# Optimization experiments

Measured on AMD Instinct MI355X. Metric: run time of the kernel, lower is better.

Reference implementation:

```python
import jax, jax.numpy as jnp
import numpy as np

R, H, E = 200000, 256, 100000  # num_relations, hidden_dim, num_hyperedges


def setup_inputs() -> dict:
    key = jax.random.key(0)
    ks = jax.random.split(key, 8)
    rng = np.random.default_rng(0)
    # ragged hyperedge sizes in [1, 15], avg ~8 -> total ~800k src entries
    sizes = rng.integers(1, 16, size=E)
    total = int(sizes.sum())
    he_ptr = jnp.asarray(np.concatenate([[0], np.cumsum(sizes)]), dtype=jnp.int64)
    he_src = jax.random.randint(ks[0], (total,), 0, R, dtype=jnp.int64)
    # unique targets make the scatter deterministic and equivalent)
    he_tgt = jnp.asarray(rng.permutation(R)[:E], dtype=jnp.int64)
    he_w = jax.random.uniform(ks[1], (E,), dtype=jnp.float32)
    x = jax.random.normal(ks[2], (R, H), dtype=jnp.float32)
    s = 1.0 / np.sqrt(H)
    W_msg = jax.random.uniform(ks[3], (H, H), jnp.float32, -s, s)
    b_msg = jnp.zeros((H,), jnp.float32)
    W_gate = jax.random.uniform(ks[4], (2 * H, H), jnp.float32, -s, s)
    b_gate = jnp.zeros((H,), jnp.float32)
    W_upd = jax.random.uniform(ks[5], (H, H), jnp.float32, -s, s)
    b_upd = jnp.zeros((H,), jnp.float32)
    return {"x": x, "he_ptr": he_ptr, "he_src": he_src, "he_tgt": he_tgt,
            "he_w": he_w, "W_msg": W_msg, "b_msg": b_msg,
            "W_gate": W_gate, "b_gate": b_gate, "W_upd": W_upd, "b_upd": b_upd}


def reference(x, he_ptr, he_src, he_tgt, he_w, W_msg, b_msg, W_gate, b_gate, W_upd, b_upd):
    total = he_src.shape[0]
    num_e = he_tgt.shape[0]
    # segment id of each src entry: which hyperedge it belongs to
    seg = jnp.searchsorted(he_ptr, jnp.arange(total), side="right") - 1
    gathered = x[he_src]                                   # [total, H]
    sums = jax.ops.segment_sum(gathered, seg, num_segments=num_e)  # [E, H]
    counts = (he_ptr[1:] - he_ptr[:-1]).astype(x.dtype)    # [E]
    src_mean = sums / counts[:, None]                      # segment mean
    msg = src_mean @ W_msg + b_msg                         # [E, H]
    tgt_x = x[he_tgt]                                      # [E, H]
    gate = jax.nn.sigmoid(jnp.concatenate([tgt_x, msg], axis=-1) @ W_gate + b_gate)
    upd = tgt_x + he_w[:, None] * gate * msg               # gated residual
    out = x.at[he_tgt].set(upd)                            # unique targets
    out = jnp.clip(out @ W_upd + b_upd, 0.0, 1.0)          # clipped relu
    return out
```

## Files before the change

### kernel.cpp

```cpp
#include <hip/hip_runtime.h>
#include <math.h>

#define H 256

typedef __attribute__((ext_vector_type(8))) short short8;
typedef __attribute__((ext_vector_type(4))) float f32x4;
typedef __attribute__((ext_vector_type(4))) int int4v;
typedef __attribute__((ext_vector_type(2))) unsigned int uint2v;
typedef unsigned short ushort_t;

__device__ __forceinline__ float bf2f(unsigned short u) {
    union { unsigned int i; float f; } v; v.i = ((unsigned int)u) << 16; return v.f;
}
__device__ __forceinline__ unsigned short f2bf(float f) {
    union { float f; unsigned int i; } v; v.f = f;
    unsigned int r = v.i + 0x7FFFu + ((v.i >> 16) & 1u);
    return (unsigned short)(r >> 16);
}
__device__ __forceinline__ void glds16(const void* g, void* l) {
    __builtin_amdgcn_global_load_lds((const __attribute__((address_space(1))) void*)g,
                                     (__attribute__((address_space(3))) void*)l, 16, 0, 0);
}
__device__ __forceinline__ int4v pack_f32x8_bf16(const float* p) {
    float4 f0 = *(const float4*)(p);
    float4 f1 = *(const float4*)(p + 4);
    int4v d;
    d.x = (int)((unsigned)f2bf(f0.x) | ((unsigned)f2bf(f0.y) << 16));
    d.y = (int)((unsigned)f2bf(f0.z) | ((unsigned)f2bf(f0.w) << 16));
    d.z = (int)((unsigned)f2bf(f1.x) | ((unsigned)f2bf(f1.y) << 16));
    d.w = (int)((unsigned)f2bf(f1.z) | ((unsigned)f2bf(f1.w) << 16));
    return d;
}

__global__ void prep_all(const float* __restrict__ Wm, const float* __restrict__ Wg,
                         const float* __restrict__ Wu, const float* __restrict__ x,
                         ushort_t* __restrict__ Wmt, ushort_t* __restrict__ Wgt,
                         ushort_t* __restrict__ Wut, int* __restrict__ imap,
                         ushort_t* __restrict__ yb, int R, size_t n8) {
    size_t gtid = (size_t)blockIdx.x * blockDim.x + threadIdx.x;
    size_t stride = (size_t)gridDim.x * blockDim.x;
    for (size_t i = gtid; i < 65536; i += stride) {
        int n = (int)(i >> 8), k = (int)(i & 255);
        Wmt[i] = f2bf(Wm[(size_t)k * 256 + n]);
        Wut[i] = f2bf(Wu[(size_t)k * 256 + n]);
    }
    for (size_t i = gtid; i < 131072; i += stride) {
        int n = (int)(i >> 9), k = (int)(i & 511);
        Wgt[i] = f2bf(Wg[(size_t)k * 256 + n]);
    }
    if (imap) for (size_t i = gtid; i < (size_t)R; i += stride) imap[i] = -1;
    if (yb) for (size_t i = gtid; i < n8; i += stride)
        *(int4v*)(yb + i * 8) = pack_f32x8_bf16(x + i * 8);
}

__global__ void imap_scatter(const int* __restrict__ tgt, int* __restrict__ imap, int E) {
    int e = blockIdx.x * 256 + threadIdx.x;
    if (e < E) imap[tgt[e]] = e;
}

__global__ __launch_bounds__(256) void seg_mean_bf16(const ushort_t* __restrict__ yb,
                                                     const int* __restrict__ ptr,
                                                     const int* __restrict__ src,
                                                     ushort_t* __restrict__ smb, int E) {
    int e = blockIdx.x * 8 + (threadIdx.x >> 5);
    if (e >= E) return;
    int lane = threadIdx.x & 31;
    const ushort_t* base = yb + lane * 8;
    int s = ptr[e], t = ptr[e + 1];
    float a0 = 0.f, a1 = 0.f, a2 = 0.f, a3 = 0.f, a4 = 0.f, a5 = 0.f, a6 = 0.f, a7 = 0.f;
    int i = s;
    for (; i + 4 <= t; i += 4) {
        int4v v0 = *(const int4v*)(base + (size_t)src[i + 0] * H);
        int4v v1 = *(const int4v*)(base + (size_t)src[i + 1] * H);
        int4v v2 = *(const int4v*)(base + (size_t)src[i + 2] * H);
        int4v v3 = *(const int4v*)(base + (size_t)src[i + 3] * H);
        a0 += bf2f((unsigned)v0.x & 0xffff) + bf2f((unsigned)v1.x & 0xffff) + bf2f((unsigned)v2.x & 0xffff) + bf2f((unsigned)v3.x & 0xffff);
        a1 += bf2f((unsigned)v0.x >> 16)    + bf2f((unsigned)v1.x >> 16)    + bf2f((unsigned)v2.x >> 16)    + bf2f((unsigned)v3.x >> 16);
        a2 += bf2f((unsigned)v0.y & 0xffff) + bf2f((unsigned)v1.y & 0xffff) + bf2f((unsigned)v2.y & 0xffff) + bf2f((unsigned)v3.y & 0xffff);
        a3 += bf2f((unsigned)v0.y >> 16)    + bf2f((unsigned)v1.y >> 16)    + bf2f((unsigned)v2.y >> 16)    + bf2f((unsigned)v3.y >> 16);
        a4 += bf2f((unsigned)v0.z & 0xffff) + bf2f((unsigned)v1.z & 0xffff) + bf2f((unsigned)v2.z & 0xffff) + bf2f((unsigned)v3.z & 0xffff);
        a5 += bf2f((unsigned)v0.z >> 16)    + bf2f((unsigned)v1.z >> 16)    + bf2f((unsigned)v2.z >> 16)    + bf2f((unsigned)v3.z >> 16);
        a6 += bf2f((unsigned)v0.w & 0xffff) + bf2f((unsigned)v1.w & 0xffff) + bf2f((unsigned)v2.w & 0xffff) + bf2f((unsigned)v3.w & 0xffff);
        a7 += bf2f((unsigned)v0.w >> 16)    + bf2f((unsigned)v1.w >> 16)    + bf2f((unsigned)v2.w >> 16)    + bf2f((unsigned)v3.w >> 16);
    }
    for (; i < t; ++i) {
        int4v v = *(const int4v*)(base + (size_t)src[i] * H);
        a0 += bf2f((unsigned)v.x & 0xffff); a1 += bf2f((unsigned)v.x >> 16);
        a2 += bf2f((unsigned)v.y & 0xffff); a3 += bf2f((unsigned)v.y >> 16);
        a4 += bf2f((unsigned)v.z & 0xffff); a5 += bf2f((unsigned)v.z >> 16);
        a6 += bf2f((unsigned)v.w & 0xffff); a7 += bf2f((unsigned)v.w >> 16);
    }
    float inv = 1.f / (float)(t - s);
    int4v o;
    o.x = (int)((unsigned)f2bf(a0 * inv) | ((unsigned)f2bf(a1 * inv) << 16));
    o.y = (int)((unsigned)f2bf(a2 * inv) | ((unsigned)f2bf(a3 * inv) << 16));
    o.z = (int)((unsigned)f2bf(a4 * inv) | ((unsigned)f2bf(a5 * inv) << 16));
    o.w = (int)((unsigned)f2bf(a6 * inv) | ((unsigned)f2bf(a7 * inv) << 16));
    *(int4v*)(smb + (size_t)e * H + lane * 8) = o;
}

__global__ __launch_bounds__(256) void seg_mean_f32w(const float* __restrict__ x,
                                                     const int* __restrict__ ptr,
                                                     const int* __restrict__ src,
                                                     ushort_t* __restrict__ smb, int E) {
    int e = blockIdx.x * 4 + (threadIdx.x >> 6);
    if (e >= E) return;
    int lane = threadIdx.x & 63;
    int s = ptr[e], t = ptr[e + 1];
    float a0 = 0.f, a1 = 0.f, a2 = 0.f, a3 = 0.f;
    int i = s;
    for (; i + 4 <= t; i += 4) {
        float4 v0 = *(const float4*)(x + (size_t)src[i + 0] * H + lane * 4);
        float4 v1 = *(const float4*)(x + (size_t)src[i + 1] * H + lane * 4);
        float4 v2 = *(const float4*)(x + (size_t)src[i + 2] * H + lane * 4);
        float4 v3 = *(const float4*)(x + (size_t)src[i + 3] * H + lane * 4);
        a0 += v0.x + v1.x + v2.x + v3.x;
        a1 += v0.y + v1.y + v2.y + v3.y;
        a2 += v0.z + v1.z + v2.z + v3.z;
        a3 += v0.w + v1.w + v2.w + v3.w;
    }
    for (; i < t; ++i) {
        float4 v = *(const float4*)(x + (size_t)src[i] * H + lane * 4);
        a0 += v.x; a1 += v.y; a2 += v.z; a3 += v.w;
    }
    float inv = 1.f / (float)(t - s);
    uint2v o;
    o.x = (unsigned)f2bf(a0 * inv) | ((unsigned)f2bf(a1 * inv) << 16);
    o.y = (unsigned)f2bf(a2 * inv) | ((unsigned)f2bf(a3 * inv) << 16);
    *(uint2v*)(smb + (size_t)e * H + lane * 4) = o;
}

#define LOADA_CHUNK_F(k0v, d)                                                            \
    do {                                                                                 \
        if constexpr (MODE == 1) {                                                       \
            if ((k0v) < 256) d = pack_f32x8_bf16(pXf + (k0v));                           \
            else             d = *(const int4v*)(pA + ((k0v) - 256));                    \
        } else {                                                                         \
            if (!useF) d = *(const int4v*)(p2 + (k0v));                                  \
            else       d = pack_f32x8_bf16(p2f + (k0v));                                 \
        }                                                                                \
    } while (0)

#define STAGE_GL(k0v, bufv)                                                              \
    do {                                                                                 \
        glds16(bSrc0 + (k0v), (char*)&Bs[bufv][0] + tid * 16);                           \
        glds16(bSrc1 + (k0v), (char*)&Bs[bufv][0] + (tid + 512) * 16);                   \
        if constexpr (MODE == 1) {                                                       \
            const ushort_t* s_ = ((k0v) < 256) ? (aP0 + (k0v)) : (aP1 + (k0v));          \
            glds16(s_, (char*)&As[bufv][0] + tid * 16);                                  \
        } else {                                                                         \
            glds16(aP0 + (k0v), (char*)&As[bufv][0] + tid * 16);                         \
        }                                                                                \
    } while (0)

#define COMPUTE_GL(bufv)                                                                 \
    do {                                                                                 \
        const char* aBase = (const char*)&As[bufv][0];                                   \
        const char* bBase = (const char*)&Bs[bufv][0];                                   \
        const int kg = lane >> 4;                                                        \
        short8 a0, a1, a2, a3;                                                           \
        int r0 = wr * 64 + (lane & 15);                                                  \
        int r1 = r0 + 16, r2 = r0 + 32, r3 = r0 + 48;                                    \
        a0 = *(const short8*)(aBase + (r0 * 4 + (kg ^ ((r0 >> 1) & 3))) * 16);           \
        a1 = *(const short8*)(aBase + (r1 * 4 + (kg ^ ((r1 >> 1) & 3))) * 16);           \
        a2 = *(const short8*)(aBase + (r2 * 4 + (kg ^ ((r2 >> 1) & 3))) * 16);           \
        a3 = *(const short8*)(aBase + (r3 * 4 + (kg ^ ((r3 >> 1) & 3))) * 16);           \
        _Pragma("unroll")                                                                \
        for (int fn = 0; fn < 4; ++fn) {                                                 \
            int cn = wc * 64 + fn * 16 + (lane & 15);                                    \
            short8 b = *(const short8*)(bBase + (cn * 4 + (kg ^ ((cn >> 1) & 3))) * 16); \
            acc[0][fn] = __builtin_amdgcn_mfma_f32_16x16x32_bf16(a0, b, acc[0][fn], 0, 0, 0); \
            acc[1][fn] = __builtin_amdgcn_mfma_f32_16x16x32_bf16(a1, b, acc[1][fn], 0, 0, 0); \
            acc[2][fn] = __builtin_amdgcn_mfma_f32_16x16x32_bf16(a2, b, acc[2][fn], 0, 0, 0); \
            acc[3][fn] = __builtin_amdgcn_mfma_f32_16x16x32_bf16(a3, b, acc[3][fn], 0, 0, 0); \
        }                                                                                \
    } while (0)

template<int MODE, int KTOT, bool XB>
__global__ __launch_bounds__(512, 4) void wgemm(
    const ushort_t* __restrict__ Abf,
    const float* __restrict__ Xf,
    const ushort_t* __restrict__ Xb,
    const ushort_t* __restrict__ Aux,
    const int* __restrict__ Idx,
    const float* __restrict__ Hew,
    const ushort_t* __restrict__ Wt,
    const float* __restrict__ Bias,
    ushort_t* __restrict__ OutB,
    float* __restrict__ OutF,
    int M)
{
    constexpr int NT = KTOT / 32;
    constexpr bool GL = (MODE == 0 || MODE == 3 || (MODE == 1 && XB));
    const int m0 = blockIdx.x * 128;
    const int tid = threadIdx.x;
    const int wv = tid >> 6;
    const int lane = tid & 63;
    const int wr = wv >> 2, wc = wv & 3;

    __shared__ __align__(16) ushort_t As[3][128 * 32];
    __shared__ __align__(16) ushort_t Bs[3][256 * 32];

    const int aRow  = tid >> 2;
    const int sl    = tid & 3;
    const int aCc   = sl ^ ((aRow >> 1) & 3);
    const int bCol0 = tid >> 2;
    const int bCol1 = bCol0 + 128;
    const int bCc0  = sl ^ ((bCol0 >> 1) & 3);
    const int bCc1  = sl ^ ((bCol1 >> 1) & 3);

    const ushort_t* bSrc0 = Wt + (size_t)bCol0 * KTOT + bCc0 * 8;
    const ushort_t* bSrc1 = Wt + (size_t)bCol1 * KTOT + bCc1 * 8;

    int r = m0 + aRow; if (r > M - 1) r = M - 1;

    const ushort_t* aP0 = nullptr;
    const ushort_t* aP1 = nullptr;
    const float* pXf = nullptr; const ushort_t* pA = nullptr;
    const ushort_t* p2 = nullptr; const float* p2f = nullptr;
    bool useF = false;
    if constexpr (MODE == 0 || MODE == 3) {
        aP0 = Abf + (size_t)r * KTOT + aCc * 8;
    } else if constexpr (MODE == 1) {
        int tr = Idx[r];
        if constexpr (XB) {
            aP0 = Xb + (size_t)tr * 256 + aCc * 8;
            aP1 = Aux + (size_t)r * 256 + aCc * 8 - 256;
        } else {
            pXf = Xf + (size_t)tr * 256 + aCc * 8;
            pA  = Aux + (size_t)r * 256 + aCc * 8;
        }
    } else {
        int e = Idx[r];
        if (e >= 0) { p2 = Aux + (size_t)e * 256 + aCc * 8; useF = false; }
        else        { p2f = Xf + (size_t)r * 256 + aCc * 8; useF = true; }
    }

    f32x4 acc[4][4];
#pragma unroll
    for (int i = 0; i < 4; ++i)
#pragma unroll
        for (int j = 0; j < 4; ++j) acc[i][j] = (f32x4){0.f, 0.f, 0.f, 0.f};

    if constexpr (GL) {
        STAGE_GL(0, 0);
        STAGE_GL(32, 1);
#pragma unroll
        for (int kt = 0; kt < NT; ++kt) {
            if (kt == NT - 1) asm volatile("s_waitcnt vmcnt(0)" ::: "memory");
            else              asm volatile("s_waitcnt vmcnt(3)" ::: "memory");
            __builtin_amdgcn_s_barrier();
            if (kt + 2 < NT) {
                const int k0 = (kt + 2) * 32;
                const int bn = (kt + 2) % 3;
                STAGE_GL(k0, bn);
            }
            COMPUTE_GL(kt % 3);
        }
    } else {
        {
            int4v d0; LOADA_CHUNK_F(0, d0);
            *(int4v*)((char*)&As[0][0] + tid * 16) = d0;
        }
        glds16(bSrc0, (char*)&Bs[0][0] + tid * 16);
        glds16(bSrc1, (char*)&Bs[0][0] + (tid + 512) * 16);
#pragma unroll 2
        for (int kt = 0; kt < NT; ++kt) {
            __syncthreads();
            const int cur = kt & 1;
            const int nxt = cur ^ 1;
            const bool more = (kt + 1 < NT);
            int4v pf;
            if (more) {
                const int k0 = (kt + 1) * 32;
                glds16(bSrc0 + k0, (char*)&Bs[nxt][0] + tid * 16);
                glds16(bSrc1 + k0, (char*)&Bs[nxt][0] + (tid + 512) * 16);
                LOADA_CHUNK_F(k0, pf);
            }
            COMPUTE_GL(cur);
            if (more) {
                *(int4v*)((char*)&As[nxt][0] + tid * 16) = pf;
            }
        }
    }

#pragma unroll
    for (int fm = 0; fm < 4; ++fm) {
        int rbase = m0 + wr * 64 + fm * 16 + (lane >> 4) * 4;
#pragma unroll
        for (int fn = 0; fn < 4; ++fn) {
            int col = wc * 64 + fn * 16 + (lane & 15);
            float bia = Bias[col];
            f32x4 v = acc[fm][fn];
#pragma unroll
            for (int i = 0; i < 4; ++i) {
                int rg = rbase + i;
                if (rg < M) {
                    float z = v[i] + bia;
                    if constexpr (MODE == 0) {
                        OutB[(size_t)rg * 256 + col] = f2bf(z);
                    } else if constexpr (MODE == 1) {
                        float g = 1.f / (1.f + __expf(-z));
                        int tr = Idx[rg];
                        float tx;
                        if constexpr (XB) tx = bf2f(Xb[(size_t)tr * 256 + col]);
                        else              tx = Xf[(size_t)tr * 256 + col];
                        float m = bf2f(Aux[(size_t)rg * 256 + col]);
                        float u = tx + Hew[rg] * g * m;
                        if constexpr (XB) OutB[(size_t)tr * 256 + col] = f2bf(u);
                        else              OutB[(size_t)rg * 256 + col] = f2bf(u);
                    } else {
                        OutF[(size_t)rg * 256 + col] = fminf(fmaxf(z, 0.f), 1.f);
                    }
                }
            }
        }
    }
}

extern "C" void kernel_launch(void* const* d_in, const int* in_sizes, int n_in,
                              void* d_out, int out_size, void* d_ws, size_t ws_size,
                              hipStream_t stream) {
    const float* x      = (const float*)d_in[0];
    const int*   he_ptr = (const int*)d_in[1];
    const int*   he_src = (const int*)d_in[2];
    const int*   he_tgt = (const int*)d_in[3];
    const float* he_w   = (const float*)d_in[4];
    const float* W_msg  = (const float*)d_in[5];
    const float* b_msg  = (const float*)d_in[6];
    const float* W_gate = (const float*)d_in[7];
    const float* b_gate = (const float*)d_in[8];
    const float* W_upd  = (const float*)d_in[9];
    const float* b_upd  = (const float*)d_in[10];

    const int E = in_sizes[3];
    const int R = in_sizes[0] / H;

    const size_t wbytes = (size_t)(65536 + 131072 + 65536) * 2;
    const size_t needA = (size_t)R * H * 2 + (size_t)E * H * 2 * 2 + (size_t)R * 4 + wbytes;
    const bool bigws = ws_size >= needA;

    const int gE = (E + 127) / 128;
    const int gR = (R + 127) / 128;

    if (bigws) {
        char* ws = (char*)d_ws;
        ushort_t* yb   = (ushort_t*)ws;
        ushort_t* buf0 = yb + (size_t)R * H;
        ushort_t* buf1 = buf0 + (size_t)E * H;
        ushort_t* Wmt  = (ushort_t*)(buf1 + (size_t)E * H);
        ushort_t* Wgt  = Wmt + 256 * 256;
        ushort_t* Wut  = Wgt + 256 * 512;

        prep_all<<<2048, 256, 0, stream>>>(W_msg, W_gate, W_upd, x,
                                           Wmt, Wgt, Wut, (int*)nullptr, yb, R, (size_t)R * H / 8);
        seg_mean_bf16<<<(E + 7) / 8, 256, 0, stream>>>(yb, he_ptr, he_src, buf0, E);

        wgemm<0, 256, true><<<gE, 512, 0, stream>>>(buf0, nullptr, yb, nullptr, nullptr, nullptr,
                                                    Wmt, b_msg, buf1, nullptr, E);
        wgemm<1, 512, true><<<gE, 512, 0, stream>>>(nullptr, nullptr, yb, buf1, he_tgt, he_w,
                                                    Wgt, b_gate, yb, nullptr, E);
        wgemm<3, 256, true><<<gR, 512, 0, stream>>>(yb, nullptr, nullptr, nullptr, nullptr, nullptr,
                                                    Wut, b_upd, nullptr, (float*)d_out, R);
    } else {
        char* ws = (char*)d_ws;
        ushort_t* buf0 = (ushort_t*)ws;
        ushort_t* buf1 = buf0 + (size_t)E * H;
        int*      imap = (int*)(buf1 + (size_t)E * H);
        ushort_t* Wmt  = (ushort_t*)((char*)imap + (size_t)R * 4);
        ushort_t* Wgt  = Wmt + 256 * 256;
        ushort_t* Wut  = Wgt + 256 * 512;

        prep_all<<<2048, 256, 0, stream>>>(W_msg, W_gate, W_upd, x,
                                           Wmt, Wgt, Wut, imap, (ushort_t*)nullptr, R, 0);
        imap_scatter<<<(E + 255) / 256, 256, 0, stream>>>(he_tgt, imap, E);
        seg_mean_f32w<<<(E + 3) / 4, 256, 0, stream>>>(x, he_ptr, he_src, buf0, E);

        wgemm<0, 256, false><<<gE, 512, 0, stream>>>(buf0, nullptr, nullptr, nullptr, nullptr, nullptr,
                                                     Wmt, b_msg, buf1, nullptr, E);
        wgemm<1, 512, false><<<gE, 512, 0, stream>>>(nullptr, x, nullptr, buf1, he_tgt, he_w,
                                                     Wgt, b_gate, buf0, nullptr, E);
        wgemm<2, 256, false><<<gR, 512, 0, stream>>>(nullptr, x, nullptr, buf0, imap, nullptr,
                                                     Wut, b_upd, nullptr, (float*)d_out, R);
    }
}
```

Before: 346.0 us.

## Fuse weight/x bf16 conversion with segment-mean gather in one launch

Merges the prep kernel (weight transpose, x-to-bf16 conversion) and the segment-mean kernel into a single launch, with the first 2048 blocks doing conversion and the rest doing the segment mean. Because the two now run concurrently, the segment mean gathers fp32 rows from x directly instead of the bf16 copy, removing the dependency and one kernel boundary. In exchange, the gather reads twice as many bytes per source row.

```diff
diff --git a/kernel.cpp b/kernel.cpp
--- a/kernel.cpp
+++ b/kernel.cpp
@@ -32,63 +32,59 @@
     return d;
 }
 
-__global__ void prep_all(const float* __restrict__ Wm, const float* __restrict__ Wg,
-                         const float* __restrict__ Wu, const float* __restrict__ x,
-                         ushort_t* __restrict__ Wmt, ushort_t* __restrict__ Wgt,
-                         ushort_t* __restrict__ Wut, int* __restrict__ imap,
-                         ushort_t* __restrict__ yb, int R, size_t n8) {
-    size_t gtid = (size_t)blockIdx.x * blockDim.x + threadIdx.x;
-    size_t stride = (size_t)gridDim.x * blockDim.x;
-    for (size_t i = gtid; i < 65536; i += stride) {
-        int n = (int)(i >> 8), k = (int)(i & 255);
-        Wmt[i] = f2bf(Wm[(size_t)k * 256 + n]);
-        Wut[i] = f2bf(Wu[(size_t)k * 256 + n]);
-    }
-    for (size_t i = gtid; i < 131072; i += stride) {
-        int n = (int)(i >> 9), k = (int)(i & 511);
-        Wgt[i] = f2bf(Wg[(size_t)k * 256 + n]);
-    }
-    if (imap) for (size_t i = gtid; i < (size_t)R; i += stride) imap[i] = -1;
-    if (yb) for (size_t i = gtid; i < n8; i += stride)
-        *(int4v*)(yb + i * 8) = pack_f32x8_bf16(x + i * 8);
-}
-
-__global__ void imap_scatter(const int* __restrict__ tgt, int* __restrict__ imap, int E) {
-    int e = blockIdx.x * 256 + threadIdx.x;
-    if (e < E) imap[tgt[e]] = e;
-}
-
-__global__ __launch_bounds__(256) void seg_mean_bf16(const ushort_t* __restrict__ yb,
-                                                     const int* __restrict__ ptr,
-                                                     const int* __restrict__ src,
-                                                     ushort_t* __restrict__ smb, int E) {
-    int e = blockIdx.x * 8 + (threadIdx.x >> 5);
+#define CONVB 2048
+
+__global__ __launch_bounds__(256) void prep_seg(
+    const float* __restrict__ Wm, const float* __restrict__ Wg,
+    const float* __restrict__ Wu, const float* __restrict__ x,
+    const int* __restrict__ ptr, const int* __restrict__ src,
+    ushort_t* __restrict__ Wmt, ushort_t* __restrict__ Wgt,
+    ushort_t* __restrict__ Wut,
+    ushort_t* __restrict__ yb, ushort_t* __restrict__ smb,
+    int R, int E, size_t n8)
+{
+    if (blockIdx.x < CONVB) {
+        size_t gtid = (size_t)blockIdx.x * 256 + threadIdx.x;
+        size_t stride = (size_t)CONVB * 256;
+        for (size_t i = gtid; i < 65536; i += stride) {
+            int n = (int)(i >> 8), k = (int)(i & 255);
+            Wmt[i] = f2bf(Wm[(size_t)k * 256 + n]);
+            Wut[i] = f2bf(Wu[(size_t)k * 256 + n]);
+        }
+        for (size_t i = gtid; i < 131072; i += stride) {
+            int n = (int)(i >> 9), k = (int)(i & 511);
+            Wgt[i] = f2bf(Wg[(size_t)k * 256 + n]);
+        }
+        for (size_t i = gtid; i < n8; i += stride)
+            *(int4v*)(yb + i * 8) = pack_f32x8_bf16(x + i * 8);
+        return;
+    }
+    int e = (blockIdx.x - CONVB) * 8 + (threadIdx.x >> 5);
     if (e >= E) return;
     int lane = threadIdx.x & 31;
-    const ushort_t* base = yb + lane * 8;
+    const float* base = x + lane * 8;
     int s = ptr[e], t = ptr[e + 1];
     float a0 = 0.f, a1 = 0.f, a2 = 0.f, a3 = 0.f, a4 = 0.f, a5 = 0.f, a6 = 0.f, a7 = 0.f;
     int i = s;
     for (; i + 4 <= t; i += 4) {
-        int4v v0 = *(const int4v*)(base + (size_t)src[i + 0] * H);
-        int4v v1 = *(const int4v*)(base + (size_t)src[i + 1] * H);
-        int4v v2 = *(const int4v*)(base + (size_t)src[i + 2] * H);
-        int4v v3 = *(const int4v*)(base + (size_t)src[i + 3] * H);
-        a0 += bf2f((unsigned)v0.x & 0xffff) + bf2f((unsigned)v1.x & 0xffff) + bf2f((unsigned)v2.x & 0xffff) + bf2f((unsigned)v3.x & 0xffff);
-        a1 += bf2f((unsigned)v0.x >> 16)    + bf2f((unsigned)v1.x >> 16)    + bf2f((unsigned)v2.x >> 16)    + bf2f((unsigned)v3.x >> 16);
-        a2 += bf2f((unsigned)v0.y & 0xffff) + bf2f((unsigned)v1.y & 0xffff) + bf2f((unsigned)v2.y & 0xffff) + bf2f((unsigned)v3.y & 0xffff);
-        a3 += bf2f((unsigned)v0.y >> 16)    + bf2f((unsigned)v1.y >> 16)    + bf2f((unsigned)v2.y >> 16)    + bf2f((unsigned)v3.y >> 16);
-        a4 += bf2f((unsigned)v0.z & 0xffff) + bf2f((unsigned)v1.z & 0xffff) + bf2f((unsigned)v2.z & 0xffff) + bf2f((unsigned)v3.z & 0xffff);
-        a5 += bf2f((unsigned)v0.z >> 16)    + bf2f((unsigned)v1.z >> 16)    + bf2f((unsigned)v2.z >> 16)    + bf2f((unsigned)v3.z >> 16);
-        a6 += bf2f((unsigned)v0.w & 0xffff) + bf2f((unsigned)v1.w & 0xffff) + bf2f((unsigned)v2.w & 0xffff) + bf2f((unsigned)v3.w & 0xffff);
-        a7 += bf2f((unsigned)v0.w >> 16)    + bf2f((unsigned)v1.w >> 16)    + bf2f((unsigned)v2.w >> 16)    + bf2f((unsigned)v3.w >> 16);
+        const float* p0 = base + (size_t)src[i + 0] * H;
+        const float* p1 = base + (size_t)src[i + 1] * H;
+        const float* p2 = base + (size_t)src[i + 2] * H;
+        const float* p3 = base + (size_t)src[i + 3] * H;
+        float4 l0 = *(const float4*)(p0), h0 = *(const float4*)(p0 + 4);
+        float4 l1 = *(const float4*)(p1), h1 = *(const float4*)(p1 + 4);
+        float4 l2 = *(const float4*)(p2), h2 = *(const float4*)(p2 + 4);
+        float4 l3 = *(const float4*)(p3), h3 = *(const float4*)(p3 + 4);
+        a0 += l0.x + l1.x + l2.x + l3.x;  a1 += l0.y + l1.y + l2.y + l3.y;
+        a2 += l0.z + l1.z + l2.z + l3.z;  a3 += l0.w + l1.w + l2.w + l3.w;
+        a4 += h0.x + h1.x + h2.x + h3.x;  a5 += h0.y + h1.y + h2.y + h3.y;
+        a6 += h0.z + h1.z + h2.z + h3.z;  a7 += h0.w + h1.w + h2.w + h3.w;
     }
     for (; i < t; ++i) {
-        int4v v = *(const int4v*)(base + (size_t)src[i] * H);
-        a0 += bf2f((unsigned)v.x & 0xffff); a1 += bf2f((unsigned)v.x >> 16);
-        a2 += bf2f((unsigned)v.y & 0xffff); a3 += bf2f((unsigned)v.y >> 16);
-        a4 += bf2f((unsigned)v.z & 0xffff); a5 += bf2f((unsigned)v.z >> 16);
-        a6 += bf2f((unsigned)v.w & 0xffff); a7 += bf2f((unsigned)v.w >> 16);
+        const float* p = base + (size_t)src[i] * H;
+        float4 lo = *(const float4*)(p), hi = *(const float4*)(p + 4);
+        a0 += lo.x; a1 += lo.y; a2 += lo.z; a3 += lo.w;
+        a4 += hi.x; a5 += hi.y; a6 += hi.z; a7 += hi.w;
     }
     float inv = 1.f / (float)(t - s);
     int4v o;
@@ -97,6 +93,29 @@
     o.z = (int)((unsigned)f2bf(a4 * inv) | ((unsigned)f2bf(a5 * inv) << 16));
     o.w = (int)((unsigned)f2bf(a6 * inv) | ((unsigned)f2bf(a7 * inv) << 16));
     *(int4v*)(smb + (size_t)e * H + lane * 8) = o;
+}
+
+__global__ void prep_all(const float* __restrict__ Wm, const float* __restrict__ Wg,
+                         const float* __restrict__ Wu,
+                         ushort_t* __restrict__ Wmt, ushort_t* __restrict__ Wgt,
+                         ushort_t* __restrict__ Wut, int* __restrict__ imap, int R) {
+    size_t gtid = (size_t)blockIdx.x * blockDim.x + threadIdx.x;
+    size_t stride = (size_t)gridDim.x * blockDim.x;
+    for (size_t i = gtid; i < 65536; i += stride) {
+        int n = (int)(i >> 8), k = (int)(i & 255);
+        Wmt[i] = f2bf(Wm[(size_t)k * 256 + n]);
+        Wut[i] = f2bf(Wu[(size_t)k * 256 + n]);
+    }
+    for (size_t i = gtid; i < 131072; i += stride) {
+        int n = (int)(i >> 9), k = (int)(i & 511);
+        Wgt[i] = f2bf(Wg[(size_t)k * 256 + n]);
+    }
+    for (size_t i = gtid; i < (size_t)R; i += stride) imap[i] = -1;
+}
+
+__global__ void imap_scatter(const int* __restrict__ tgt, int* __restrict__ imap, int E) {
+    int e = blockIdx.x * 256 + threadIdx.x;
+    if (e < E) imap[tgt[e]] = e;
 }
 
 __global__ __launch_bounds__(256) void seg_mean_f32w(const float* __restrict__ x,
@@ -352,9 +371,9 @@
         ushort_t* Wgt  = Wmt + 256 * 256;
         ushort_t* Wut  = Wgt + 256 * 512;
 
-        prep_all<<<2048, 256, 0, stream>>>(W_msg, W_gate, W_upd, x,
-                                           Wmt, Wgt, Wut, (int*)nullptr, yb, R, (size_t)R * H / 8);
-        seg_mean_bf16<<<(E + 7) / 8, 256, 0, stream>>>(yb, he_ptr, he_src, buf0, E);
+        prep_seg<<<CONVB + (E + 7) / 8, 256, 0, stream>>>(
+            W_msg, W_gate, W_upd, x, he_ptr, he_src,
+            Wmt, Wgt, Wut, yb, buf0, R, E, (size_t)R * H / 8);
 
         wgemm<0, 256, true><<<gE, 512, 0, stream>>>(buf0, nullptr, yb, nullptr, nullptr, nullptr,
                                                     Wmt, b_msg, buf1, nullptr, E);
@@ -371,8 +390,7 @@
         ushort_t* Wgt  = Wmt + 256 * 256;
         ushort_t* Wut  = Wgt + 256 * 512;
 
-        prep_all<<<2048, 256, 0, stream>>>(W_msg, W_gate, W_upd, x,
-                                           Wmt, Wgt, Wut, imap, (ushort_t*)nullptr, R, 0);
+        prep_all<<<2048, 256, 0, stream>>>(W_msg, W_gate, W_upd, Wmt, Wgt, Wut, imap, R);
         imap_scatter<<<(E + 255) / 256, 256, 0, stream>>>(he_tgt, imap, E);
         seg_mean_f32w<<<(E + 3) / 4, 256, 0, stream>>>(x, he_ptr, he_src, buf0, E);
 
```

Result: slower. 407.3 us (+17.7%).
